# Performance work log

Measured on AMD Instinct MI355X. Metric: run time of the kernel, lower is better.

The kernel has to match this reference:

```python
import jax, jax.numpy as jnp
import numpy as np

N_NODES = 100000
N_EDGES = 1600000
N_GRAPHS = 1000
NODES_PER_GRAPH = 100
D_IN = 128
D_HID = 128
N_TASKS = 12


def setup_inputs() -> dict:
    key = jax.random.key(0)
    ks = jax.random.split(key, 6)
    X = jax.random.normal(ks[0], (N_NODES, D_IN), dtype=jnp.float32)
    edge_index = jax.random.randint(ks[1], (2, N_EDGES), 0, N_NODES, dtype=jnp.int64)
    graph_sizes = jnp.full((N_GRAPHS,), NODES_PER_GRAPH, dtype=jnp.int64)  # sums to N_NODES
    s0 = (2.0 / D_IN) ** 0.5
    W0 = jax.random.normal(ks[2], (D_IN, D_HID), dtype=jnp.float32) * s0
    b0 = jnp.zeros((D_HID,), dtype=jnp.float32)
    W1 = jax.random.normal(ks[3], (D_HID, D_HID), dtype=jnp.float32) * s0
    b1 = jnp.zeros((D_HID,), dtype=jnp.float32)
    Wf = jax.random.normal(ks[4], (D_HID, N_TASKS), dtype=jnp.float32) * s0
    bf = jnp.zeros((N_TASKS,), dtype=jnp.float32)
    return {"X": X, "edge_index": edge_index, "graph_sizes": graph_sizes,
            "W0": W0, "b0": b0, "W1": W1, "b1": b1, "Wf": Wf, "bf": bf}


def reference(X, edge_index, graph_sizes, W0, b0, W1, b1, Wf, bf):
    src, dst = edge_index[0], edge_index[1]
    n = X.shape[0]

    def gconv(x, W, b):
        # GCN-style message passing with self term: sum_{j->i} (x_j W) + x_i W + b
        xw = x @ W                                                    # [N, d]
        agg = jax.ops.segment_sum(xw[src], dst, num_segments=n)       # [N, d]
        return agg + xw + b

    # stacked conv -> relu -> dropout(eval=identity)
    h = jax.nn.relu(gconv(X, W0, b0))
    h = jax.nn.relu(gconv(h, W1, b1))
    out = jax.nn.sigmoid(h @ Wf + bf)                                  # [N, T]

    # ragged per-graph mean readout as a single segment-mean
    g = graph_sizes.shape[0]
    seg_ids = jnp.repeat(jnp.arange(g), graph_sizes, total_repeat_length=n)
    sums = jax.ops.segment_sum(out, seg_ids, num_segments=g)           # [G, T]
    return sums / graph_sizes[:, None].astype(out.dtype)
```

## Files before the change

kernel.cpp:

```cpp
#include <hip/hip_runtime.h>
#include <math.h>

#define D 128
#define NBUCK_MAX 1024
#define NB_EDGE   256
#define CAPSEG    40
#define CAPB      4096
#define CAPE      2600

typedef unsigned short u16;
typedef unsigned int   u32;
typedef __attribute__((ext_vector_type(8))) short short8;
typedef __attribute__((ext_vector_type(4))) float f32x4;
typedef __attribute__((ext_vector_type(2))) float f32x2;

static __device__ __forceinline__ u16 f32_to_bf16(float f) {
    u32 u = __builtin_bit_cast(u32, f);
    u32 r = (u + 0x7FFFu + ((u >> 16) & 1u)) >> 16;
    return (u16)r;
}
static __device__ __forceinline__ u32 pack_bf16x2(float lo, float hi) {
    return (u32)f32_to_bf16(lo) | ((u32)f32_to_bf16(hi) << 16);
}
static __device__ __forceinline__ float bf16lo_to_f32(u32 v) {
    return __builtin_bit_cast(float, v << 16);
}
static __device__ __forceinline__ float bf16hi_to_f32(u32 v) {
    return __builtin_bit_cast(float, v & 0xFFFF0000u);
}

__global__ __launch_bounds__(512) void prep_place(const int* __restrict__ src, const int* __restrict__ dst,
                                                  int E, int nbuck,
                                                  u32* __restrict__ edgeBuf, int* __restrict__ segCount,
                                                  const float* __restrict__ W0, const float* __restrict__ W1,
                                                  u16* __restrict__ Wp0, u16* __restrict__ Wp1,
                                                  const float* __restrict__ Wf, float* __restrict__ Wfp,
                                                  const int* __restrict__ gsz, int G, int* __restrict__ goff) {
    const int b = blockIdx.x;
    const int tid = threadIdx.x;
    if (b < NB_EDGE) {
        __shared__ int cur[NBUCK_MAX];
        for (int i = tid; i < nbuck; i += 512) cur[i] = 0;
        __syncthreads();
        int per = (E + NB_EDGE - 1) / NB_EDGE;
        int s = b * per, e = min(E, s + per);
        for (int i = s + tid; i < e; i += 512) {
            int d = dst[i];
            int bk = d >> 7;
            int pos = atomicAdd(&cur[bk], 1);
            if (pos < CAPSEG)
                edgeBuf[((size_t)bk * NB_EDGE + b) * CAPSEG + pos] = (u32)src[i] | ((u32)(d & 127) << 20);
        }
        __syncthreads();
        for (int i = tid; i < nbuck; i += 512) segCount[b * nbuck + i] = min(cur[i], CAPSEG);
    } else if (b == NB_EDGE) {
        __shared__ int wsum[8];
        int base = tid * 4;
        int v[4];
        #pragma unroll
        for (int k = 0; k < 4; k++) v[k] = (base + k < G) ? gsz[base + k] : 0;
        int s = v[0] + v[1] + v[2] + v[3];
        int lane = tid & 63;
        int incl = s;
        #pragma unroll
        for (int off = 1; off < 64; off <<= 1) { int t = __shfl_up(incl, off); if (lane >= off) incl += t; }
        int wv = tid >> 6;
        if (lane == 63) wsum[wv] = incl;
        __syncthreads();
        int woff = 0;
        for (int w = 0; w < wv; w++) woff += wsum[w];
        int run = woff + incl - s;
        #pragma unroll
        for (int k = 0; k < 4; k++) {
            if (base + k <= G) goff[base + k] = run;
            run += v[k];
        }
    } else if (b == NB_EDGE + 1) {
        for (int i = tid; i < 64 * 24; i += 512) {
            int lane = i / 24, r = i % 24, k = r / 3, j = r % 3;
            Wfp[i] = Wf[(((lane & 15) * 8) + k) * 12 + 3 * (lane >> 4) + j];
        }
    } else {
        int gidx = (b - (NB_EDGE + 2)) * 512 + tid;
        const float* W = (gidx < 128 * 128) ? W0 : W1;
        u16* Wp = (gidx < 128 * 128) ? Wp0 : Wp1;
        int idx = gidx & (128 * 128 - 1);
        int j = idx & 7, lane = (idx >> 3) & 63, kt = (idx >> 9) & 3, nt = idx >> 11;
        int k = kt * 32 + ((lane >> 4) << 3) + j;
        int n = nt * 16 + (lane & 15);
        Wp[idx] = f32_to_bf16(W[k * 128 + n]);
    }
}

static __device__ __forceinline__ void gemm_body(const short8 af[4], const u16* __restrict__ Wp,
                                                 u16* __restrict__ outb, int N, int row0,
                                                 int tid, int wave, int lane, int quad, int l16,
                                                 u16* Cs) {
    f32x4 acc[8];
    #pragma unroll
    for (int nt = 0; nt < 8; nt++) acc[nt] = (f32x4){0.f, 0.f, 0.f, 0.f};
    #pragma unroll
    for (int kt = 0; kt < 4; kt++) {
        #pragma unroll
        for (int nt = 0; nt < 8; nt++) {
            short8 bf = *(const short8*)(Wp + ((size_t)(nt * 4 + kt) * 64 + lane) * 8);
            acc[nt] = __builtin_amdgcn_mfma_f32_16x16x32_bf16(af[kt], bf, acc[nt], 0, 0, 0);
        }
    }
    #pragma unroll
    for (int nt = 0; nt < 8; nt++) {
        #pragma unroll
        for (int r = 0; r < 4; r++) {
            int rl = wave * 16 + quad * 4 + r;
            Cs[rl * 136 + nt * 16 + l16] = f32_to_bf16(acc[nt][r]);
        }
    }
    __syncthreads();
    for (int i = tid; i < 64 * 16; i += 256) {
        int row = i >> 4, chunk = i & 15;
        int grow = row0 + row;
        if (grow <= N)
            *(uint4*)(outb + (size_t)grow * 128 + chunk * 8) =
                *(const uint4*)(Cs + row * 136 + chunk * 8);
    }
}

__global__ __launch_bounds__(256) void finalize_gemm0(const u32* __restrict__ edgeBuf,
                                                      const int* __restrict__ segCount,
                                                      int2* __restrict__ rowse, int* __restrict__ col_idx,
                                                      int nbuck,
                                                      const float* __restrict__ A, const u16* __restrict__ Wp,
                                                      u16* __restrict__ outb, int N) {
    __shared__ u16 Cs[64 * 136];
    const int tid = threadIdx.x;
    if ((int)blockIdx.x < nbuck) {
        int* iCs   = (int*)Cs;
        u32* eL    = (u32*)iCs;
        int* hist  = iCs + CAPE;
        int* lcur  = iCs + CAPE + 128;
        int* scnt  = iCs + CAPE + 256;
        int* sbase = iCs + CAPE + 512;
        const int b = blockIdx.x;
        const size_t ebase = (size_t)b * NB_EDGE * CAPSEG;
        for (int i = tid; i < NB_EDGE; i += 256) scnt[i] = segCount[i * nbuck + b];
        if (tid < 128) hist[tid] = 0;
        __syncthreads();
        if (tid < 64) {
            int carry = 0;
            #pragma unroll
            for (int c4 = 0; c4 < NB_EDGE / 64; c4++) {
                int v = scnt[c4 * 64 + tid];
                int incl = v;
                #pragma unroll
                for (int off = 1; off < 64; off <<= 1) { int t = __shfl_up(incl, off); if (tid >= off) incl += t; }
                sbase[c4 * 64 + tid] = carry + incl - v;
                carry += __shfl(incl, 63);
            }
            if (tid == 0) sbase[NB_EDGE] = carry;
        }
        __syncthreads();
        const int nE = min(sbase[NB_EDGE], CAPE);
        for (int p = tid; p < nE; p += 256) {
            int lo = 0, hi = NB_EDGE;
            #pragma unroll
            for (int s = 0; s < 8; s++) {
                int mid = (lo + hi) >> 1;
                if (sbase[mid] <= p) lo = mid; else hi = mid;
            }
            eL[p] = edgeBuf[ebase + (size_t)lo * CAPSEG + (p - sbase[lo])];
        }
        __syncthreads();
        for (int i = tid; i < nE; i += 256)
            atomicAdd(&hist[(int)(eL[i] >> 20)], 1);
        __syncthreads();
        if (tid < 64) {
            int v0 = hist[tid * 2], v1 = hist[tid * 2 + 1];
            int s = v0 + v1;
            int incl = s;
            #pragma unroll
            for (int off = 1; off < 64; off <<= 1) { int t = __shfl_up(incl, off); if (tid >= off) incl += t; }
            int excl = incl - s;
            lcur[tid * 2] = excl;
            lcur[tid * 2 + 1] = excl + v0;
            int node = b * 128 + tid * 2;
            int st = b * CAPB + excl;
            if (node < N) rowse[node] = make_int2(st, st + v0);
            if (node + 1 < N) rowse[node + 1] = make_int2(st + v0, st + v0 + v1);
        }
        __syncthreads();
        for (int i = tid; i < nE; i += 256) {
            u32 p = eL[i];
            int pos = atomicAdd(&lcur[p >> 20], 1);
            col_idx[b * CAPB + pos] = (int)(p & 0xFFFFFu);
        }
    } else {
        const int bid = blockIdx.x - nbuck;
        const int wave = tid >> 6, lane = tid & 63, quad = lane >> 4, l16 = lane & 15;
        const int row0 = bid * 64;
        const int arow = row0 + wave * 16 + l16;
        union { u32 u[4]; short8 s; } cv;
        short8 af[4];
        if (arow < N) {
            const float* ab = A + (size_t)arow * 128 + quad * 8;
            #pragma unroll
            for (int kt = 0; kt < 4; kt++) {
                float4 x0 = *(const float4*)(ab + kt * 32);
                float4 x1 = *(const float4*)(ab + kt * 32 + 4);
                cv.u[0] = pack_bf16x2(x0.x, x0.y);
                cv.u[1] = pack_bf16x2(x0.z, x0.w);
                cv.u[2] = pack_bf16x2(x1.x, x1.y);
                cv.u[3] = pack_bf16x2(x1.z, x1.w);
                af[kt] = cv.s;
            }
        } else {
            short8 z = {0, 0, 0, 0, 0, 0, 0, 0};
            #pragma unroll
            for (int kt = 0; kt < 4; kt++) af[kt] = z;
        }
        gemm_body(af, Wp, outb, N, row0, tid, wave, lane, quad, l16, Cs);
    }
}

static __device__ __forceinline__ void add_row(f32x2* acc, uint4 u) {
    acc[0] += (f32x2){bf16lo_to_f32(u.x), bf16hi_to_f32(u.x)};
    acc[1] += (f32x2){bf16lo_to_f32(u.y), bf16hi_to_f32(u.y)};
    acc[2] += (f32x2){bf16lo_to_f32(u.z), bf16hi_to_f32(u.z)};
    acc[3] += (f32x2){bf16lo_to_f32(u.w), bf16hi_to_f32(u.w)};
}

static __device__ __forceinline__ void gather_core(const u16* __restrict__ xwb, const int2* __restrict__ rowse,
                                                   const int* __restrict__ col_idx, const float* __restrict__ bias,
                                                   int wid, int lane, int N, int q, int d8, float r[8]) {
    f32x2 acc[4];
    #pragma unroll
    for (int t = 0; t < 4; t++) acc[t] = (f32x2){0.f, 0.f};
    int2 se = rowse[wid];
    int start = se.x, end = se.y;
    for (int e = start; e < end; e += 64) {
        int idx = e + lane;
        int j = (idx < end) ? col_idx[idx] : N;
        int cnt = min(64, end - e);
        for (int i = 0; i < cnt; i += 16) {
            int j0 = __shfl(j, i + q);
            int j1 = __shfl(j, i + 4 + q);
            int j2 = __shfl(j, i + 8 + q);
            int j3 = __shfl(j, i + 12 + q);
            uint4 r0 = *(const uint4*)(xwb + (size_t)j0 * D + d8);
            uint4 r1 = *(const uint4*)(xwb + (size_t)j1 * D + d8);
            uint4 r2 = *(const uint4*)(xwb + (size_t)j2 * D + d8);
            uint4 r3 = *(const uint4*)(xwb + (size_t)j3 * D + d8);
            add_row(acc, r0);
            add_row(acc, r1);
            add_row(acc, r2);
            add_row(acc, r3);
        }
    }
    float av[8] = {acc[0].x, acc[0].y, acc[1].x, acc[1].y, acc[2].x, acc[2].y, acc[3].x, acc[3].y};
    #pragma unroll
    for (int t = 0; t < 8; t++) {
        av[t] += __shfl_xor(av[t], 16);
        av[t] += __shfl_xor(av[t], 32);
    }
    uint4 sv = *(const uint4*)(xwb + (size_t)wid * D + d8);
    float4 ba = *(const float4*)(bias + d8);
    float4 bb = *(const float4*)(bias + d8 + 4);
    r[0] = fmaxf(av[0] + bf16lo_to_f32(sv.x) + ba.x, 0.f);
    r[1] = fmaxf(av[1] + bf16hi_to_f32(sv.x) + ba.y, 0.f);
    r[2] = fmaxf(av[2] + bf16lo_to_f32(sv.y) + ba.z, 0.f);
    r[3] = fmaxf(av[3] + bf16hi_to_f32(sv.y) + ba.w, 0.f);
    r[4] = fmaxf(av[4] + bf16lo_to_f32(sv.z) + bb.x, 0.f);
    r[5] = fmaxf(av[5] + bf16hi_to_f32(sv.z) + bb.y, 0.f);
    r[6] = fmaxf(av[6] + bf16lo_to_f32(sv.w) + bb.z, 0.f);
    r[7] = fmaxf(av[7] + bf16hi_to_f32(sv.w) + bb.w, 0.f);
}

__global__ __launch_bounds__(256) void agg_gemm1(const u16* __restrict__ xwb, const int2* __restrict__ rowse,
                                                 const int* __restrict__ col_idx, const float* __restrict__ bias,
                                                 const u16* __restrict__ Wp, u16* __restrict__ outb, int N) {
    __shared__ u16 hs[16 * 136];
    __shared__ u16 Cs[16 * 136];
    const int tid = threadIdx.x;
    const int wave = tid >> 6, lane = tid & 63, quad = lane >> 4, l16 = lane & 15;
    const int tile = blockIdx.x * 16;
    const int d8 = l16 * 8;
    #pragma unroll
    for (int m = 0; m < 4; m++) {
        int nodeLocal = wave * 4 + m;
        int wid = tile + nodeLocal;
        if (wid < N) {
            float r[8];
            gather_core(xwb, rowse, col_idx, bias, wid, lane, N, quad, d8, r);
            if (quad == 0) {
                uint4 o;
                o.x = pack_bf16x2(r[0], r[1]);
                o.y = pack_bf16x2(r[2], r[3]);
                o.z = pack_bf16x2(r[4], r[5]);
                o.w = pack_bf16x2(r[6], r[7]);
                *(uint4*)(hs + nodeLocal * 136 + d8) = o;
            }
        } else if (quad == 0) {
            *(uint4*)(hs + nodeLocal * 136 + d8) = make_uint4(0, 0, 0, 0);
        }
    }
    __syncthreads();
    short8 af[4];
    #pragma unroll
    for (int kt = 0; kt < 4; kt++)
        af[kt] = *(const short8*)(hs + l16 * 136 + kt * 32 + quad * 8);
    f32x4 acc[2];
    acc[0] = (f32x4){0.f, 0.f, 0.f, 0.f};
    acc[1] = (f32x4){0.f, 0.f, 0.f, 0.f};
    #pragma unroll
    for (int kt = 0; kt < 4; kt++) {
        #pragma unroll
        for (int t = 0; t < 2; t++) {
            int nt = wave * 2 + t;
            short8 bf = *(const short8*)(Wp + ((size_t)(nt * 4 + kt) * 64 + lane) * 8);
            acc[t] = __builtin_amdgcn_mfma_f32_16x16x32_bf16(af[kt], bf, acc[t], 0, 0, 0);
        }
    }
    #pragma unroll
    for (int t = 0; t < 2; t++) {
        int nt = wave * 2 + t;
        #pragma unroll
        for (int r = 0; r < 4; r++)
            Cs[(quad * 4 + r) * 136 + nt * 16 + l16] = f32_to_bf16(acc[t][r]);
    }
    __syncthreads();
    {
        int row = tid >> 4, chunk = tid & 15;
        int grow = tile + row;
        if (grow <= N)
            *(uint4*)(outb + (size_t)grow * 128 + chunk * 8) =
                *(const uint4*)(Cs + row * 136 + chunk * 8);
    }
}

__global__ __launch_bounds__(256) void agg_head(const u16* __restrict__ xwb, const int2* __restrict__ rowse,
                                                const int* __restrict__ col_idx, const float* __restrict__ bias,
                                                const float* __restrict__ Wfp, const float* __restrict__ bfv,
                                                float* __restrict__ out12, int N) {
    int wid = (blockIdx.x * 256 + threadIdx.x) >> 6;
    int lane = threadIdx.x & 63;
    if (wid >= N) return;
    const int q = lane >> 4;
    const int d8 = (lane & 15) * 8;
    float w[24];
    const float* wp = Wfp + lane * 24;
    #pragma unroll
    for (int i = 0; i < 6; i++) *(float4*)(w + i * 4) = *(const float4*)(wp + i * 4);
    float r[8];
    gather_core(xwb, rowse, col_idx, bias, wid, lane, N, q, d8, r);
    const int t0 = 3 * q;
    float p0 = 0.f, p1 = 0.f, p2 = 0.f;
    #pragma unroll
    for (int k = 0; k < 8; k++) {
        p0 += r[k] * w[k * 3];
        p1 += r[k] * w[k * 3 + 1];
        p2 += r[k] * w[k * 3 + 2];
    }
    #pragma unroll
    for (int m = 1; m <= 8; m <<= 1) {
        p0 += __shfl_xor(p0, m);
        p1 += __shfl_xor(p1, m);
        p2 += __shfl_xor(p2, m);
    }
    if ((lane & 15) == 0) {
        float s0 = 1.f / (1.f + __expf(-(p0 + bfv[t0])));
        float s1 = 1.f / (1.f + __expf(-(p1 + bfv[t0 + 1])));
        float s2 = 1.f / (1.f + __expf(-(p2 + bfv[t0 + 2])));
        float* o = out12 + (size_t)wid * 12 + t0;
        o[0] = s0; o[1] = s1; o[2] = s2;
    }
}

__global__ __launch_bounds__(128) void graph_mean(const float* __restrict__ out12, const int* __restrict__ goff,
                                                  float* __restrict__ out, int G) {
    __shared__ float partial[120];
    int g = blockIdx.x;
    int tid = threadIdx.x;
    int start = goff[g];
    int size = goff[g + 1] - start;
    if (tid < 120) {
        int t = tid % 12, chunk = tid / 12;
        float s = 0.f;
        for (int i = chunk; i < size; i += 10)
            s += out12[(size_t)(start + i) * 12 + t];
        partial[tid] = s;
    }
    __syncthreads();
    if (tid < 12) {
        float tot = 0.f;
        #pragma unroll
        for (int c = 0; c < 10; c++) tot += partial[c * 12 + tid];
        out[(size_t)g * 12 + tid] = tot / (float)size;
    }
}


extern "C" void kernel_launch(void* const* d_in, const int* in_sizes, int n_in,
                              void* d_out, int out_size, void* d_ws, size_t ws_size,
                              hipStream_t stream) {
    const float* X   = (const float*)d_in[0];
    const int* edges = (const int*)d_in[1];
    const int* gsz   = (const int*)d_in[2];
    const float* W0  = (const float*)d_in[3];
    const float* b0  = (const float*)d_in[4];
    const float* W1  = (const float*)d_in[5];
    const float* b1  = (const float*)d_in[6];
    const float* Wf  = (const float*)d_in[7];
    const float* bfv = (const float*)d_in[8];
    float* out = (float*)d_out;

    const int N = in_sizes[0] / D;
    const int E = in_sizes[1] / 2;
    const int G = in_sizes[2];
    const int* esrc = edges;
    const int* edst = edges + E;
    const int nbuck = (N + 127) >> 7;

    char* ws = (char*)d_ws;
    char* p = ws;
    u16* xwb     = (u16*)p;  p += (((size_t)(N + 64) * D * 2) + 255) & ~255ull;
    u16* hb      = (u16*)p;  p += (((size_t)(N + 64) * D * 2) + 255) & ~255ull;
    u16* Wp0     = (u16*)p;  p += ((size_t)128 * 128 * 2 + 255) & ~255ull;
    u16* Wp1     = (u16*)p;  p += ((size_t)128 * 128 * 2 + 255) & ~255ull;
    float* Wfp   = (float*)p; p += ((size_t)64 * 24 * 4 + 255) & ~255ull;
    u32* edgeBuf = (u32*)p;  p += (((size_t)nbuck * NB_EDGE * CAPSEG * 4) + 255) & ~255ull;
    int* segCount = (int*)p; p += (((size_t)NB_EDGE * NBUCK_MAX * 4) + 255) & ~255ull;
    int* col_idx = (int*)p;  p += (((size_t)nbuck * CAPB * 4) + 255) & ~255ull;
    int2* rowse  = (int2*)p; p += (((size_t)N * 8) + 255) & ~255ull;
    float* out12 = (float*)p; p += (((size_t)N * 12 * 4) + 255) & ~255ull;
    int* goff    = (int*)p;

    prep_place<<<NB_EDGE + 2 + 64, 512, 0, stream>>>(esrc, edst, E, nbuck, edgeBuf, segCount,
                                                     W0, W1, Wp0, Wp1, Wf, Wfp, gsz, G, goff);
    const int gemmGrid = (N + 63) / 64;
    finalize_gemm0<<<nbuck + gemmGrid, 256, 0, stream>>>(edgeBuf, segCount, rowse, col_idx, nbuck,
                                                         X, Wp0, xwb, N);
    agg_gemm1<<<N / 16 + 1, 256, 0, stream>>>(xwb, rowse, col_idx, b0, Wp1, hb, N);
    agg_head<<<(N * 64 + 255) / 256, 256, 0, stream>>>(hb, rowse, col_idx, b1, Wfp, bfv, out12, N);
    graph_mean<<<G, 128, 0, stream>>>(out12, goff, out, G);
}
```

Measured before the change: 279.9 us.

## Fold self-loops into CSR and gather two nodes per wave

The CSR build now reserves one slot per node for the node itself, so the self term is read through the same neighbour gather as the edges instead of as a separate row load. The aggregation is restructured so each wave processes two destination nodes at once, interleaving their neighbour loads to keep more memory requests in flight. Rows with more than 64 entries fall back to a non-inlined tail routine. In exchange, register pressure rises, and the head kernel launches half as many waves, which may reduce occupancy or load balance.

After: 368.8 us. +31.8%, slower.

```diff
diff --git a/kernel.cpp b/kernel.cpp
--- a/kernel.cpp
+++ b/kernel.cpp
@@ -180,12 +180,14 @@
             #pragma unroll
             for (int off = 1; off < 64; off <<= 1) { int t = __shfl_up(incl, off); if (tid >= off) incl += t; }
             int excl = incl - s;
-            lcur[tid * 2] = excl;
-            lcur[tid * 2 + 1] = excl + v0;
+            int le0 = excl + tid * 2;
+            int le1 = le0 + v0 + 1;
+            lcur[tid * 2]     = le0 + 1;
+            lcur[tid * 2 + 1] = le1 + 1;
             int node = b * 128 + tid * 2;
-            int st = b * CAPB + excl;
-            if (node < N) rowse[node] = make_int2(st, st + v0);
-            if (node + 1 < N) rowse[node + 1] = make_int2(st + v0, st + v0 + v1);
+            int st0 = b * CAPB + le0, st1 = b * CAPB + le1;
+            if (node < N)     { rowse[node]     = make_int2(st0, st1);          col_idx[st0] = node; }
+            if (node + 1 < N) { rowse[node + 1] = make_int2(st1, st1 + v1 + 1); col_idx[st1] = node + 1; }
         }
         __syncthreads();
         for (int i = tid; i < nE; i += 256) {
@@ -228,50 +230,95 @@
     acc[3] += (f32x2){bf16lo_to_f32(u.w), bf16hi_to_f32(u.w)};
 }
 
-static __device__ __forceinline__ void gather_core(const u16* __restrict__ xwb, const int2* __restrict__ rowse,
-                                                   const int* __restrict__ col_idx, const float* __restrict__ bias,
-                                                   int wid, int lane, int N, int q, int d8, float r[8]) {
-    f32x2 acc[4];
-    #pragma unroll
-    for (int t = 0; t < 4; t++) acc[t] = (f32x2){0.f, 0.f};
-    int2 se = rowse[wid];
-    int start = se.x, end = se.y;
-    for (int e = start; e < end; e += 64) {
-        int idx = e + lane;
-        int j = (idx < end) ? col_idx[idx] : N;
-        int cnt = min(64, end - e);
-        for (int i = 0; i < cnt; i += 16) {
-            int j0 = __shfl(j, i + q);
-            int j1 = __shfl(j, i + 4 + q);
-            int j2 = __shfl(j, i + 8 + q);
-            int j3 = __shfl(j, i + 12 + q);
-            uint4 r0 = *(const uint4*)(xwb + (size_t)j0 * D + d8);
-            uint4 r1 = *(const uint4*)(xwb + (size_t)j1 * D + d8);
-            uint4 r2 = *(const uint4*)(xwb + (size_t)j2 * D + d8);
-            uint4 r3 = *(const uint4*)(xwb + (size_t)j3 * D + d8);
-            add_row(acc, r0);
-            add_row(acc, r1);
-            add_row(acc, r2);
-            add_row(acc, r3);
-        }
-    }
-    float av[8] = {acc[0].x, acc[0].y, acc[1].x, acc[1].y, acc[2].x, acc[2].y, acc[3].x, acc[3].y};
+static __device__ __attribute__((noinline)) void tail_batch(f32x2 acc[4], const u16* __restrict__ xwb,
+                                                            const int* __restrict__ col_idx,
+                                                            int e, int end, int lane, int N, int q, int d8) {
+    int idx = e + lane;
+    int j = (idx < end) ? col_idx[idx] : N;
+    int cnt = min(64, end - e);
+    for (int i = 0; i < cnt; i += 16) {
+        int j0 = __shfl(j, i + q);
+        int j1 = __shfl(j, i + 4 + q);
+        int j2 = __shfl(j, i + 8 + q);
+        int j3 = __shfl(j, i + 12 + q);
+        add_row(acc, *(const uint4*)(xwb + (size_t)j0 * D + d8));
+        add_row(acc, *(const uint4*)(xwb + (size_t)j1 * D + d8));
+        add_row(acc, *(const uint4*)(xwb + (size_t)j2 * D + d8));
+        add_row(acc, *(const uint4*)(xwb + (size_t)j3 * D + d8));
+    }
+}
+
+static __device__ __forceinline__ void gather2(const u16* __restrict__ xwb, const int2* __restrict__ rowse,
+                                               const int* __restrict__ col_idx, const float* __restrict__ bias,
+                                               int wid0, int wid1, int lane, int N, int q, int d8,
+                                               float r0[8], float r1[8]) {
+    f32x2 accA[4], accB[4];
+    #pragma unroll
+    for (int t = 0; t < 4; t++) { accA[t] = (f32x2){0.f, 0.f}; accB[t] = (f32x2){0.f, 0.f}; }
+    int2 seA = rowse[wid0];
+    int2 seB = rowse[wid1];
+    int ia = seA.x + lane, ib = seB.x + lane;
+    int jA = (ia < seA.y) ? col_idx[ia] : N;
+    int jB = (ib < seB.y) ? col_idx[ib] : N;
+    int cntA = min(64, seA.y - seA.x);
+    int cntB = min(64, seB.y - seB.x);
+    int mx = max(cntA, cntB);
+    for (int i = 0; i < mx; i += 16) {
+        int a0 = __shfl(jA, i + q);
+        int a1 = __shfl(jA, i + 4 + q);
+        int a2 = __shfl(jA, i + 8 + q);
+        int a3 = __shfl(jA, i + 12 + q);
+        int b0 = __shfl(jB, i + q);
+        int b1 = __shfl(jB, i + 4 + q);
+        int b2 = __shfl(jB, i + 8 + q);
+        int b3 = __shfl(jB, i + 12 + q);
+        uint4 ra0 = *(const uint4*)(xwb + (size_t)a0 * D + d8);
+        uint4 ra1 = *(const uint4*)(xwb + (size_t)a1 * D + d8);
+        uint4 ra2 = *(const uint4*)(xwb + (size_t)a2 * D + d8);
+        uint4 ra3 = *(const uint4*)(xwb + (size_t)a3 * D + d8);
+        uint4 rb0 = *(const uint4*)(xwb + (size_t)b0 * D + d8);
+        uint4 rb1 = *(const uint4*)(xwb + (size_t)b1 * D + d8);
+        uint4 rb2 = *(const uint4*)(xwb + (size_t)b2 * D + d8);
+        uint4 rb3 = *(const uint4*)(xwb + (size_t)b3 * D + d8);
+        add_row(accA, ra0);
+        add_row(accA, ra1);
+        add_row(accA, ra2);
+        add_row(accA, ra3);
+        add_row(accB, rb0);
+        add_row(accB, rb1);
+        add_row(accB, rb2);
+        add_row(accB, rb3);
+    }
+    for (int e = seA.x + 64; e < seA.y; e += 64) tail_batch(accA, xwb, col_idx, e, seA.y, lane, N, q, d8);
+    for (int e = seB.x + 64; e < seB.y; e += 64) tail_batch(accB, xwb, col_idx, e, seB.y, lane, N, q, d8);
+
+    float av0[8] = {accA[0].x, accA[0].y, accA[1].x, accA[1].y, accA[2].x, accA[2].y, accA[3].x, accA[3].y};
+    float av1[8] = {accB[0].x, accB[0].y, accB[1].x, accB[1].y, accB[2].x, accB[2].y, accB[3].x, accB[3].y};
     #pragma unroll
     for (int t = 0; t < 8; t++) {
-        av[t] += __shfl_xor(av[t], 16);
-        av[t] += __shfl_xor(av[t], 32);
-    }
-    uint4 sv = *(const uint4*)(xwb + (size_t)wid * D + d8);
+        av0[t] += __shfl_xor(av0[t], 16);
+        av0[t] += __shfl_xor(av0[t], 32);
+        av1[t] += __shfl_xor(av1[t], 16);
+        av1[t] += __shfl_xor(av1[t], 32);
+    }
     float4 ba = *(const float4*)(bias + d8);
     float4 bb = *(const float4*)(bias + d8 + 4);
-    r[0] = fmaxf(av[0] + bf16lo_to_f32(sv.x) + ba.x, 0.f);
-    r[1] = fmaxf(av[1] + bf16hi_to_f32(sv.x) + ba.y, 0.f);
-    r[2] = fmaxf(av[2] + bf16lo_to_f32(sv.y) + ba.z, 0.f);
-    r[3] = fmaxf(av[3] + bf16hi_to_f32(sv.y) + ba.w, 0.f);
-    r[4] = fmaxf(av[4] + bf16lo_to_f32(sv.z) + bb.x, 0.f);
-    r[5] = fmaxf(av[5] + bf16hi_to_f32(sv.z) + bb.y, 0.f);
-    r[6] = fmaxf(av[6] + bf16lo_to_f32(sv.w) + bb.z, 0.f);
-    r[7] = fmaxf(av[7] + bf16hi_to_f32(sv.w) + bb.w, 0.f);
+    r0[0] = fmaxf(av0[0] + ba.x, 0.f);
+    r0[1] = fmaxf(av0[1] + ba.y, 0.f);
+    r0[2] = fmaxf(av0[2] + ba.z, 0.f);
+    r0[3] = fmaxf(av0[3] + ba.w, 0.f);
+    r0[4] = fmaxf(av0[4] + bb.x, 0.f);
+    r0[5] = fmaxf(av0[5] + bb.y, 0.f);
+    r0[6] = fmaxf(av0[6] + bb.z, 0.f);
+    r0[7] = fmaxf(av0[7] + bb.w, 0.f);
+    r1[0] = fmaxf(av1[0] + ba.x, 0.f);
+    r1[1] = fmaxf(av1[1] + ba.y, 0.f);
+    r1[2] = fmaxf(av1[2] + ba.z, 0.f);
+    r1[3] = fmaxf(av1[3] + ba.w, 0.f);
+    r1[4] = fmaxf(av1[4] + bb.x, 0.f);
+    r1[5] = fmaxf(av1[5] + bb.y, 0.f);
+    r1[6] = fmaxf(av1[6] + bb.z, 0.f);
+    r1[7] = fmaxf(av1[7] + bb.w, 0.f);
 }
 
 __global__ __launch_bounds__(256) void agg_gemm1(const u16* __restrict__ xwb, const int2* __restrict__ rowse,
@@ -284,22 +331,28 @@
     const int tile = blockIdx.x * 16;
     const int d8 = l16 * 8;
     #pragma unroll
-    for (int m = 0; m < 4; m++) {
-        int nodeLocal = wave * 4 + m;
-        int wid = tile + nodeLocal;
-        if (wid < N) {
-            float r[8];
-            gather_core(xwb, rowse, col_idx, bias, wid, lane, N, quad, d8, r);
-            if (quad == 0) {
-                uint4 o;
-                o.x = pack_bf16x2(r[0], r[1]);
-                o.y = pack_bf16x2(r[2], r[3]);
-                o.z = pack_bf16x2(r[4], r[5]);
-                o.w = pack_bf16x2(r[6], r[7]);
-                *(uint4*)(hs + nodeLocal * 136 + d8) = o;
-            }
-        } else if (quad == 0) {
-            *(uint4*)(hs + nodeLocal * 136 + d8) = make_uint4(0, 0, 0, 0);
+    for (int m = 0; m < 4; m += 2) {
+        int nl0 = wave * 4 + m, nl1 = nl0 + 1;
+        int wid0 = tile + nl0, wid1 = tile + nl1;
+        float r0[8], r1[8];
+        int g0 = min(wid0, N - 1), g1 = min(wid1, N - 1);
+        gather2(xwb, rowse, col_idx, bias, g0, g1, lane, N, quad, d8, r0, r1);
+        if (quad == 0) {
+            uint4 o0, o1;
+            if (wid0 < N) {
+                o0.x = pack_bf16x2(r0[0], r0[1]);
+                o0.y = pack_bf16x2(r0[2], r0[3]);
+                o0.z = pack_bf16x2(r0[4], r0[5]);
+                o0.w = pack_bf16x2(r0[6], r0[7]);
+            } else o0 = make_uint4(0, 0, 0, 0);
+            if (wid1 < N) {
+                o1.x = pack_bf16x2(r1[0], r1[1]);
+                o1.y = pack_bf16x2(r1[2], r1[3]);
+                o1.z = pack_bf16x2(r1[4], r1[5]);
+                o1.w = pack_bf16x2(r1[6], r1[7]);
+            } else o1 = make_uint4(0, 0, 0, 0);
+            *(uint4*)(hs + nl0 * 136 + d8) = o0;
+            *(uint4*)(hs + nl1 * 136 + d8) = o1;
         }
     }
     __syncthreads();
@@ -340,37 +393,52 @@
                                                 const int* __restrict__ col_idx, const float* __restrict__ bias,
                                                 const float* __restrict__ Wfp, const float* __restrict__ bfv,
                                                 float* __restrict__ out12, int N) {
-    int wid = (blockIdx.x * 256 + threadIdx.x) >> 6;
+    int wpair = (blockIdx.x * 256 + threadIdx.x) >> 6;
+    int wid0 = wpair * 2;
+    if (wid0 >= N) return;
+    int wid1 = min(wid0 + 1, N - 1);
     int lane = threadIdx.x & 63;
-    if (wid >= N) return;
     const int q = lane >> 4;
     const int d8 = (lane & 15) * 8;
     float w[24];
     const float* wp = Wfp + lane * 24;
     #pragma unroll
     for (int i = 0; i < 6; i++) *(float4*)(w + i * 4) = *(const float4*)(wp + i * 4);
-    float r[8];
-    gather_core(xwb, rowse, col_idx, bias, wid, lane, N, q, d8, r);
+    float r0[8], r1[8];
+    gather2(xwb, rowse, col_idx, bias, wid0, wid1, lane, N, q, d8, r0, r1);
     const int t0 = 3 * q;
-    float p0 = 0.f, p1 = 0.f, p2 = 0.f;
+    float p00 = 0.f, p01 = 0.f, p02 = 0.f;
+    float p10 = 0.f, p11 = 0.f, p12 = 0.f;
     #pragma unroll
     for (int k = 0; k < 8; k++) {
-        p0 += r[k] * w[k * 3];
-        p1 += r[k] * w[k * 3 + 1];
-        p2 += r[k] * w[k * 3 + 2];
+        p00 += r0[k] * w[k * 3];
+        p01 += r0[k] * w[k * 3 + 1];
+        p02 += r0[k] * w[k * 3 + 2];
+        p10 += r1[k] * w[k * 3];
+        p11 += r1[k] * w[k * 3 + 1];
+        p12 += r1[k] * w[k * 3 + 2];
     }
     #pragma unroll
     for (int m = 1; m <= 8; m <<= 1) {
-        p0 += __shfl_xor(p0, m);
-        p1 += __shfl_xor(p1, m);
-        p2 += __shfl_xor(p2, m);
+        p00 += __shfl_xor(p00, m);
+        p01 += __shfl_xor(p01, m);
+        p02 += __shfl_xor(p02, m);
+        p10 += __shfl_xor(p10, m);
+        p11 += __shfl_xor(p11, m);
+        p12 += __shfl_xor(p12, m);
     }
     if ((lane & 15) == 0) {
-        float s0 = 1.f / (1.f + __expf(-(p0 + bfv[t0])));
-        float s1 = 1.f / (1.f + __expf(-(p1 + bfv[t0 + 1])));
-        float s2 = 1.f / (1.f + __expf(-(p2 + bfv[t0 + 2])));
-        float* o = out12 + (size_t)wid * 12 + t0;
-        o[0] = s0; o[1] = s1; o[2] = s2;
+        float b0 = bfv[t0], b1 = bfv[t0 + 1], b2 = bfv[t0 + 2];
+        float* o0 = out12 + (size_t)wid0 * 12 + t0;
+        o0[0] = 1.f / (1.f + __expf(-(p00 + b0)));
+        o0[1] = 1.f / (1.f + __expf(-(p01 + b1)));
+        o0[2] = 1.f / (1.f + __expf(-(p02 + b2)));
+        if (wid0 + 1 < N) {
+            float* o1 = out12 + (size_t)wid1 * 12 + t0;
+            o1[0] = 1.f / (1.f + __expf(-(p10 + b0)));
+            o1[1] = 1.f / (1.f + __expf(-(p11 + b1)));
+            o1[2] = 1.f / (1.f + __expf(-(p12 + b2)));
+        }
     }
 }
 
@@ -439,6 +507,7 @@
     finalize_gemm0<<<nbuck + gemmGrid, 256, 0, stream>>>(edgeBuf, segCount, rowse, col_idx, nbuck,
                                                          X, Wp0, xwb, N);
     agg_gemm1<<<N / 16 + 1, 256, 0, stream>>>(xwb, rowse, col_idx, b0, Wp1, hb, N);
-    agg_head<<<(N * 64 + 255) / 256, 256, 0, stream>>>(hb, rowse, col_idx, b1, Wfp, bfv, out12, N);
+    const int waves2 = (N + 1) / 2;
+    agg_head<<<(waves2 + 3) / 4, 256, 0, stream>>>(hb, rowse, col_idx, b1, Wfp, bfv, out12, N);
     graph_mean<<<G, 128, 0, stream>>>(out12, goff, out, G);
 }
```
